# Kernel tuning notes

Hardware: AMD Instinct MI355X
Metric: run time of the kernel (lower is better)

Reference implementation:

```python
import jax, jax.numpy as jnp
import numpy as np

L = 512
INPUT = 1024
HIDDEN = 2048
VOCAB = 50257


def setup_inputs() -> dict:
    key = jax.random.key(0)
    ks = jax.random.split(key, 16)
    s_in = 1.0 / np.sqrt(INPUT)
    s_h = 1.0 / np.sqrt(HIDDEN)
    s_v = 1.0 / np.sqrt(VOCAB)
    f32 = jnp.float32
    return {
        "src": jax.random.normal(ks[0], (L, INPUT), f32),
        "tgt": jax.random.normal(ks[1], (L, INPUT), f32),
        # encoder LSTMCell params (torch layout: [4H, in], gate order i,f,g,o)
        "W_ih_e": jax.random.uniform(ks[2], (4 * HIDDEN, INPUT), f32, -s_h, s_h),
        "W_hh_e": jax.random.uniform(ks[3], (4 * HIDDEN, HIDDEN), f32, -s_h, s_h),
        "b_ih_e": jax.random.uniform(ks[4], (4 * HIDDEN,), f32, -s_h, s_h),
        "b_hh_e": jax.random.uniform(ks[5], (4 * HIDDEN,), f32, -s_h, s_h),
        # decoder LSTMCell params
        "W_ih_d": jax.random.uniform(ks[6], (4 * HIDDEN, INPUT), f32, -s_h, s_h),
        "W_hh_d": jax.random.uniform(ks[7], (4 * HIDDEN, HIDDEN), f32, -s_h, s_h),
        "b_ih_d": jax.random.uniform(ks[8], (4 * HIDDEN,), f32, -s_h, s_h),
        "b_hh_d": jax.random.uniform(ks[9], (4 * HIDDEN,), f32, -s_h, s_h),
        # fc_out: hidden -> vocab
        "W_out": jax.random.uniform(ks[10], (VOCAB, HIDDEN), f32, -s_h, s_h),
        "b_out": jax.random.uniform(ks[11], (VOCAB,), f32, -s_h, s_h),
        # fc_input_size: vocab -> input (computed per-step in original; unused under teacher forcing)
        "W_in": jax.random.uniform(ks[12], (INPUT, VOCAB), f32, -s_v, s_v),
        "b_in": jax.random.uniform(ks[13], (INPUT,), f32, -s_v, s_v),
    }


def _lstm_cell(x, h, c, W_ih, W_hh, b_ih, b_hh):
    # torch LSTMCell: gates split in order i, f, g, o
    gates = W_ih @ x + b_ih + W_hh @ h + b_hh  # [4H]
    i, f, g, o = jnp.split(gates, 4)
    i = jax.nn.sigmoid(i)
    f = jax.nn.sigmoid(f)
    g = jnp.tanh(g)
    o = jax.nn.sigmoid(o)
    c_new = f * c + i * g
    h_new = o * jnp.tanh(c_new)
    return h_new, c_new


def reference(src, tgt, W_ih_e, W_hh_e, b_ih_e, b_hh_e,
              W_ih_d, W_hh_d, b_ih_d, b_hh_d, W_out, b_out, W_in, b_in):
    H = W_hh_e.shape[1]

    # Encoder: run LSTMCell over src, keep final (h, c) as memory.
    def enc_step(carry, x):
        h, c = carry
        h, c = _lstm_cell(x, h, c, W_ih_e, W_hh_e, b_ih_e, b_hh_e)
        return (h, c), None

    h0 = jnp.zeros((H,), src.dtype)
    c0 = jnp.zeros((H,), src.dtype)
    memory, _ = jax.lax.scan(enc_step, (h0, c0), src)

    # Decoder (teacher forcing, free_running_rate=0.0): input is always tgt[i].
    def dec_step(carry, x):
        h, c = carry
        h, c = _lstm_cell(x, h, c, W_ih_d, W_hh_d, b_ih_d, b_hh_d)
        out = W_out @ h + b_out  # [vocab]
        return (h, c), out

    _, y = jax.lax.scan(dec_step, memory, tgt)  # [L, vocab]
    return y
```

## Files before the change

### kernel.cpp

```cpp
#include <hip/hip_runtime.h>

#define LSEQ 512
#define NIN 1024
#define NH 2048
#define NV 50257
#define NG 8192

typedef float f32x4 __attribute__((ext_vector_type(4)));
typedef short s16x8 __attribute__((ext_vector_type(8)));
typedef unsigned long long u64;

__device__ __forceinline__ unsigned short bf16_hi_rne(float x)
{
    unsigned u = __float_as_uint(x);
    return (unsigned short)((u + 0x7fffu + ((u >> 16) & 1u)) >> 16);
}

__global__ __launch_bounds__(256, 2)
void gemm_mfma_abT(const float* __restrict__ A, const float* __restrict__ B,
                   const float* __restrict__ bias1, const float* __restrict__ bias2,
                   float* __restrict__ C, int M, int N, int K)
{
    __shared__ unsigned short Ah[128 * 40], Al[128 * 40];
    __shared__ unsigned short Bh[128 * 40], Bl[128 * 40];

    const int tid  = threadIdx.x;
    const int m0   = blockIdx.x * 128;
    const int n0   = blockIdx.y * 128;
    const int lrow = tid >> 1;
    const int lk0  = (tid & 1) << 4;
    const int lane = tid & 63;
    const int wave = tid >> 6;
    const int wm   = (wave >> 1) * 64;
    const int wn   = (wave & 1) * 64;
    const int fr   = lane & 15;
    const int fk   = (lane >> 4) * 8;

    f32x4 acc[4][4];
#pragma unroll
    for (int i = 0; i < 4; ++i)
#pragma unroll
        for (int j = 0; j < 4; ++j) acc[i][j] = (f32x4){0.f, 0.f, 0.f, 0.f};

    const bool bvalid = (n0 + lrow) < N;
    const float* pa = A + (size_t)(m0 + lrow) * K + lk0;
    const float* pb = bvalid ? (B + (size_t)(n0 + lrow) * K + lk0) : nullptr;

    for (int k0 = 0; k0 < K; k0 += 32) {
        float4 va[4], vb[4];
#pragma unroll
        for (int q = 0; q < 4; ++q) va[q] = *(const float4*)(pa + k0 + 4 * q);
        if (bvalid) {
#pragma unroll
            for (int q = 0; q < 4; ++q) vb[q] = *(const float4*)(pb + k0 + 4 * q);
        } else {
#pragma unroll
            for (int q = 0; q < 4; ++q) vb[q] = make_float4(0.f, 0.f, 0.f, 0.f);
        }

#pragma unroll
        for (int q = 0; q < 4; ++q) {
            const float av[4] = {va[q].x, va[q].y, va[q].z, va[q].w};
            const float bv[4] = {vb[q].x, vb[q].y, vb[q].z, vb[q].w};
            ushort4 ah, alo, bh, blo;
            unsigned short* ahp = (unsigned short*)&ah;
            unsigned short* alp = (unsigned short*)&alo;
            unsigned short* bhp = (unsigned short*)&bh;
            unsigned short* blp = (unsigned short*)&blo;
#pragma unroll
            for (int j = 0; j < 4; ++j) {
                const unsigned short h = bf16_hi_rne(av[j]);
                ahp[j] = h;
                alp[j] = bf16_hi_rne(av[j] - __uint_as_float((unsigned)h << 16));
                const unsigned short g = bf16_hi_rne(bv[j]);
                bhp[j] = g;
                blp[j] = bf16_hi_rne(bv[j] - __uint_as_float((unsigned)g << 16));
            }
            const int sidx = lrow * 40 + lk0 + 4 * q;
            *(ushort4*)&Ah[sidx] = ah;
            *(ushort4*)&Al[sidx] = alo;
            *(ushort4*)&Bh[sidx] = bh;
            *(ushort4*)&Bl[sidx] = blo;
        }
        __syncthreads();

        s16x8 fah[4], fal[4], fbh[4], fbl[4];
#pragma unroll
        for (int i = 0; i < 4; ++i) {
            const int ar = (wm + i * 16 + fr) * 40 + fk;
            fah[i] = *(const s16x8*)&Ah[ar];
            fal[i] = *(const s16x8*)&Al[ar];
            const int br = (wn + i * 16 + fr) * 40 + fk;
            fbh[i] = *(const s16x8*)&Bh[br];
            fbl[i] = *(const s16x8*)&Bl[br];
        }
#pragma unroll
        for (int i = 0; i < 4; ++i)
#pragma unroll
            for (int j = 0; j < 4; ++j) {
                acc[i][j] = __builtin_amdgcn_mfma_f32_16x16x32_bf16(fah[i], fbh[j], acc[i][j], 0, 0, 0);
                acc[i][j] = __builtin_amdgcn_mfma_f32_16x16x32_bf16(fah[i], fbl[j], acc[i][j], 0, 0, 0);
                acc[i][j] = __builtin_amdgcn_mfma_f32_16x16x32_bf16(fal[i], fbh[j], acc[i][j], 0, 0, 0);
            }
        __syncthreads();
    }

    const int rbase = (lane >> 4) * 4;
#pragma unroll
    for (int j = 0; j < 4; ++j) {
        const int col = n0 + wn + j * 16 + fr;
        if (col >= N) continue;
        const float bb = bias1[col] + (bias2 ? bias2[col] : 0.f);
#pragma unroll
        for (int i = 0; i < 4; ++i) {
#pragma unroll
            for (int r = 0; r < 4; ++r) {
                const int row = m0 + wm + i * 16 + rbase + r;
                C[(size_t)row * N + col] = acc[i][j][r] + bb;
            }
        }
    }
}

__device__ __forceinline__ float sigmoidf_(float x)
{
    return 1.f / (1.f + __expf(-x));
}

__device__ __forceinline__ void tag_wait4(const u64* p0, const u64* p1,
                                          const u64* p2, const u64* p3,
                                          unsigned want, float* o)
{
    u64 a = __hip_atomic_load(p0, __ATOMIC_RELAXED, __HIP_MEMORY_SCOPE_AGENT);
    u64 b = __hip_atomic_load(p1, __ATOMIC_RELAXED, __HIP_MEMORY_SCOPE_AGENT);
    u64 c = __hip_atomic_load(p2, __ATOMIC_RELAXED, __HIP_MEMORY_SCOPE_AGENT);
    u64 d = __hip_atomic_load(p3, __ATOMIC_RELAXED, __HIP_MEMORY_SCOPE_AGENT);
    while (((unsigned)(a >> 32) != want) | ((unsigned)(b >> 32) != want) |
           ((unsigned)(c >> 32) != want) | ((unsigned)(d >> 32) != want)) {
        __builtin_amdgcn_s_sleep(1);
        a = __hip_atomic_load(p0, __ATOMIC_RELAXED, __HIP_MEMORY_SCOPE_AGENT);
        b = __hip_atomic_load(p1, __ATOMIC_RELAXED, __HIP_MEMORY_SCOPE_AGENT);
        c = __hip_atomic_load(p2, __ATOMIC_RELAXED, __HIP_MEMORY_SCOPE_AGENT);
        d = __hip_atomic_load(p3, __ATOMIC_RELAXED, __HIP_MEMORY_SCOPE_AGENT);
    }
    o[0] = __uint_as_float((unsigned)a);
    o[1] = __uint_as_float((unsigned)b);
    o[2] = __uint_as_float((unsigned)c);
    o[3] = __uint_as_float((unsigned)d);
}

#define W_LIST(F) F(0) F(1) F(2) F(3) F(4) F(5) F(6) F(7) F(8) F(9) F(10) F(11) \
  F(12) F(13) F(14) F(15) F(16) F(17) F(18) F(19) F(20) F(21) F(22) F(23) \
  F(24) F(25) F(26) F(27) F(28) F(29) F(30) F(31)
#define DECLW(I) f32x4 w##I;
#define LOADW(I) w##I = wp4[I];
#define PINW(I)  asm volatile("" : "+v"(w##I));

#define CHUNK(CH, WA, WB, WC, WD) do { \
    const f32x4 ha = *(const f32x4*)&h_s[hbase + (CH) * 16 + 0]; \
    const f32x4 hcb = *(const f32x4*)&h_s[hbase + (CH) * 16 + 4]; \
    const f32x4 hcc = *(const f32x4*)&h_s[hbase + (CH) * 16 + 8]; \
    const f32x4 hcd = *(const f32x4*)&h_s[hbase + (CH) * 16 + 12]; \
    p0 = fmaf(WA.x, ha.x, p0);  p0 = fmaf(WA.y, ha.y, p0); \
    p0 = fmaf(WA.z, ha.z, p0);  p0 = fmaf(WA.w, ha.w, p0); \
    p1 = fmaf(WB.x, hcb.x, p1); p1 = fmaf(WB.y, hcb.y, p1); \
    p1 = fmaf(WB.z, hcb.z, p1); p1 = fmaf(WB.w, hcb.w, p1); \
    p2 = fmaf(WC.x, hcc.x, p2); p2 = fmaf(WC.y, hcc.y, p2); \
    p2 = fmaf(WC.z, hcc.z, p2); p2 = fmaf(WC.w, hcc.w, p2); \
    p3 = fmaf(WD.x, hcd.x, p3); p3 = fmaf(WD.y, hcd.y, p3); \
    p3 = fmaf(WD.z, hcd.z, p3); p3 = fmaf(WD.w, hcd.w, p3); \
} while (0)

#define STEP(XP, T, GS, LAST, STOREHD) do { \
    float xc = 0.f; \
    if (sub == 0) xc = (XP)[(size_t)(T) * NG + grow];   \
    { \
        const u64* hsrc = hbq + ((GS) & 1) * NH; \
        float hv[4]; \
        tag_wait4(&hsrc[tid], &hsrc[tid + 512], &hsrc[tid + 1024], &hsrc[tid + 1536], \
                  (unsigned)((GS) + 1), hv); \
        h_s[tid          + ((tid          >> 7) << 2)] = hv[0]; \
        h_s[(tid +  512) + (((tid +  512) >> 7) << 2)] = hv[1]; \
        h_s[(tid + 1024) + (((tid + 1024) >> 7) << 2)] = hv[2]; \
        h_s[(tid + 1536) + (((tid + 1536) >> 7) << 2)] = hv[3]; \
    } \
    __syncthreads(); \
    float p0 = 0.f, p1 = 0.f, p2 = 0.f, p3 = 0.f; \
    CHUNK(0, w0, w1, w2, w3);     CHUNK(1, w4, w5, w6, w7); \
    CHUNK(2, w8, w9, w10, w11);   CHUNK(3, w12, w13, w14, w15); \
    CHUNK(4, w16, w17, w18, w19); CHUNK(5, w20, w21, w22, w23); \
    CHUNK(6, w24, w25, w26, w27); CHUNK(7, w28, w29, w30, w31); \
    float partial = (p0 + p1) + (p2 + p3); \
    partial += __shfl_xor(partial, 1); \
    partial += __shfl_xor(partial, 2); \
    partial += __shfl_xor(partial, 4); \
    partial += __shfl_xor(partial, 8); \
    if (sub == 0) gates_s[row] = partial + xc; \
    __syncthreads(); \
    if (tid < 8) { \
        const float ig = sigmoidf_(gates_s[tid]); \
        const float fg = sigmoidf_(gates_s[8 + tid]); \
        const float gg = tanhf(gates_s[16 + tid]); \
        const float og = sigmoidf_(gates_s[24 + tid]); \
        const float cn = fg * c_s[tid] + ig * gg; \
        c_s[tid] = cn; \
        const float hn = og * tanhf(cn); \
        if (STOREHD) Hd[(size_t)(T) * NH + wg * 8 + tid] = hn; \
        if (!(LAST)) { \
            const u64 pv = ((u64)(unsigned)((GS) + 2) << 32) | (u64)__float_as_uint(hn); \
            __hip_atomic_store(&hbq[(((GS) + 1) & 1) * NH + wg * 8 + tid], pv, \
                               __ATOMIC_RELAXED, __HIP_MEMORY_SCOPE_AGENT); \
        } \
    } \
} while (0)

__global__ __launch_bounds__(512, 2)
void seq_lstm(const float* __restrict__ Whh_e,
              const float* __restrict__ Whh_d,
              const float* __restrict__ Xe,
              const float* __restrict__ Xd,
              u64* __restrict__ hbq,
              float* __restrict__ Hd)
{
    const int wg   = blockIdx.x;
    const int tid  = threadIdx.x;
    const int lane = tid & 63;
    const int wv   = tid >> 6;
    const int row  = (wv << 2) + (lane >> 4);
    const int sub  = lane & 15;
    const int gate = row >> 3;
    const int u    = row & 7;
    const int grow = gate * NH + wg * 8 + u;
    const int hbase = sub * 132;

    __shared__ float h_s[2112];
    __shared__ float gates_s[32];
    __shared__ float c_s[8];

    W_LIST(DECLW)

    {
        const f32x4* wp4 = (const f32x4*)(Whh_e + (size_t)grow * NH + sub * 128);
        W_LIST(LOADW)
        W_LIST(PINW)
    }

    if (tid < 8) {
        c_s[tid] = 0.f;
        const u64 v0 = ((u64)1 << 32);
        __hip_atomic_store(&hbq[wg * 8 + tid], v0,
                           __ATOMIC_RELAXED, __HIP_MEMORY_SCOPE_AGENT);
    }
    __syncthreads();

#pragma unroll 1
    for (int t = 0; t < LSEQ; ++t) {
        STEP(Xe, t, t, false, false);
    }

    {
        const f32x4* wp4 = (const f32x4*)(Whh_d + (size_t)grow * NH + sub * 128);
        W_LIST(LOADW)
        W_LIST(PINW)
    }

#pragma unroll 1
    for (int t = 0; t < LSEQ; ++t) {
        STEP(Xd, t, LSEQ + t, (t == LSEQ - 1), true);
    }
}

extern "C" void kernel_launch(void* const* d_in, const int* in_sizes, int n_in,
                              void* d_out, int out_size, void* d_ws, size_t ws_size,
                              hipStream_t stream)
{
    const float* src   = (const float*)d_in[0];
    const float* tgt   = (const float*)d_in[1];
    const float* Wih_e = (const float*)d_in[2];
    const float* Whh_e = (const float*)d_in[3];
    const float* bih_e = (const float*)d_in[4];
    const float* bhh_e = (const float*)d_in[5];
    const float* Wih_d = (const float*)d_in[6];
    const float* Whh_d = (const float*)d_in[7];
    const float* bih_d = (const float*)d_in[8];
    const float* bhh_d = (const float*)d_in[9];
    const float* Wout  = (const float*)d_in[10];
    const float* bout  = (const float*)d_in[11];
    float* out = (float*)d_out;

    char* ws = (char*)d_ws;
    u64*  hbq = (u64*)ws;
    float* Hd = (float*)(ws + 32768);
    float* Xe = (float*)(ws + 32768 + (size_t)LSEQ * NH * 4);
    float* Xd = Xe + (size_t)LSEQ * NG;

    hipMemsetAsync(ws, 0, 32768, stream);

    const dim3 blk(256);
    gemm_mfma_abT<<<dim3(LSEQ / 128, NG / 128), blk, 0, stream>>>(
        src, Wih_e, bih_e, bhh_e, Xe, LSEQ, NG, NIN);
    gemm_mfma_abT<<<dim3(LSEQ / 128, NG / 128), blk, 0, stream>>>(
        tgt, Wih_d, bih_d, bhh_d, Xd, LSEQ, NG, NIN);

    seq_lstm<<<dim3(256), dim3(512), 0, stream>>>(
        Whh_e, Whh_d, Xe, Xd, hbq, Hd);

    gemm_mfma_abT<<<dim3(LSEQ / 128, (NV + 127) / 128), blk, 0, stream>>>(
        Hd, Wout, bout, nullptr, out, LSEQ, NV, NH);
}
```

Measured before the change: 3.212 ms.

## Remap rows so each wave owns one hidden unit, drop second barrier per step

Rows are remapped so each wavefront holds all four gates (i,f,g,o) of a single hidden unit. The gate nonlinearities are then computed in-wave through shuffles, with the cell state kept in a register instead of shared memory. This removes the gates_s shared-memory round trip and the second __syncthreads per recurrent step. The h staging buffer in LDS is double-buffered by step parity so the next step's writes cannot race with current reads, at the cost of twice the LDS and redundant activation math across lanes.

```diff
diff --git a/kernel.cpp b/kernel.cpp
--- a/kernel.cpp
+++ b/kernel.cpp
@@ -157,10 +157,10 @@
 #define PINW(I)  asm volatile("" : "+v"(w##I));
 
 #define CHUNK(CH, WA, WB, WC, WD) do { \
-    const f32x4 ha = *(const f32x4*)&h_s[hbase + (CH) * 16 + 0]; \
-    const f32x4 hcb = *(const f32x4*)&h_s[hbase + (CH) * 16 + 4]; \
-    const f32x4 hcc = *(const f32x4*)&h_s[hbase + (CH) * 16 + 8]; \
-    const f32x4 hcd = *(const f32x4*)&h_s[hbase + (CH) * 16 + 12]; \
+    const f32x4 ha = *(const f32x4*)&hb_s[hbase + (CH) * 16 + 0]; \
+    const f32x4 hcb = *(const f32x4*)&hb_s[hbase + (CH) * 16 + 4]; \
+    const f32x4 hcc = *(const f32x4*)&hb_s[hbase + (CH) * 16 + 8]; \
+    const f32x4 hcd = *(const f32x4*)&hb_s[hbase + (CH) * 16 + 12]; \
     p0 = fmaf(WA.x, ha.x, p0);  p0 = fmaf(WA.y, ha.y, p0); \
     p0 = fmaf(WA.z, ha.z, p0);  p0 = fmaf(WA.w, ha.w, p0); \
     p1 = fmaf(WB.x, hcb.x, p1); p1 = fmaf(WB.y, hcb.y, p1); \
@@ -172,19 +172,20 @@
 } while (0)
 
 #define STEP(XP, T, GS, LAST, STOREHD) do { \
-    float xc = 0.f; \
-    if (sub == 0) xc = (XP)[(size_t)(T) * NG + grow];   \
+    const float xc = (XP)[(size_t)(T) * NG + qg * NH + idx_u];  \
     { \
         const u64* hsrc = hbq + ((GS) & 1) * NH; \
         float hv[4]; \
         tag_wait4(&hsrc[tid], &hsrc[tid + 512], &hsrc[tid + 1024], &hsrc[tid + 1536], \
                   (unsigned)((GS) + 1), hv); \
-        h_s[tid          + ((tid          >> 7) << 2)] = hv[0]; \
-        h_s[(tid +  512) + (((tid +  512) >> 7) << 2)] = hv[1]; \
-        h_s[(tid + 1024) + (((tid + 1024) >> 7) << 2)] = hv[2]; \
-        h_s[(tid + 1536) + (((tid + 1536) >> 7) << 2)] = hv[3]; \
+        float* hst = h_s + ((GS) & 1) * 2112; \
+        hst[tid          + ((tid          >> 7) << 2)] = hv[0]; \
+        hst[(tid +  512) + (((tid +  512) >> 7) << 2)] = hv[1]; \
+        hst[(tid + 1024) + (((tid + 1024) >> 7) << 2)] = hv[2]; \
+        hst[(tid + 1536) + (((tid + 1536) >> 7) << 2)] = hv[3]; \
     } \
     __syncthreads(); \
+    const float* hb_s = h_s + ((GS) & 1) * 2112; \
     float p0 = 0.f, p1 = 0.f, p2 = 0.f, p3 = 0.f; \
     CHUNK(0, w0, w1, w2, w3);     CHUNK(1, w4, w5, w6, w7); \
     CHUNK(2, w8, w9, w10, w11);   CHUNK(3, w12, w13, w14, w15); \
@@ -195,20 +196,22 @@
     partial += __shfl_xor(partial, 2); \
     partial += __shfl_xor(partial, 4); \
     partial += __shfl_xor(partial, 8); \
-    if (sub == 0) gates_s[row] = partial + xc; \
-    __syncthreads(); \
-    if (tid < 8) { \
-        const float ig = sigmoidf_(gates_s[tid]); \
-        const float fg = sigmoidf_(gates_s[8 + tid]); \
-        const float gg = tanhf(gates_s[16 + tid]); \
-        const float og = sigmoidf_(gates_s[24 + tid]); \
-        const float cn = fg * c_s[tid] + ig * gg; \
-        c_s[tid] = cn; \
-        const float hn = og * tanhf(cn); \
-        if (STOREHD) Hd[(size_t)(T) * NH + wg * 8 + tid] = hn; \
+    const float gv = partial + xc; \
+    const float vi = __shfl(gv, sub,      64); \
+    const float vf = __shfl(gv, sub + 16, 64); \
+    const float vg = __shfl(gv, sub + 32, 64); \
+    const float vo = __shfl(gv, sub + 48, 64); \
+    const float ig = sigmoidf_(vi); \
+    const float fg = sigmoidf_(vf); \
+    const float gg = tanhf(vg); \
+    const float og = sigmoidf_(vo); \
+    c_reg = fg * c_reg + ig * gg; \
+    const float hn = og * tanhf(c_reg); \
+    if (lane == 0) { \
+        if (STOREHD) Hd[(size_t)(T) * NH + idx_u] = hn; \
         if (!(LAST)) { \
             const u64 pv = ((u64)(unsigned)((GS) + 2) << 32) | (u64)__float_as_uint(hn); \
-            __hip_atomic_store(&hbq[(((GS) + 1) & 1) * NH + wg * 8 + tid], pv, \
+            __hip_atomic_store(&hbq[(((GS) + 1) & 1) * NH + idx_u], pv, \
                                __ATOMIC_RELAXED, __HIP_MEMORY_SCOPE_AGENT); \
         } \
     } \
@@ -222,33 +225,30 @@
               u64* __restrict__ hbq,
               float* __restrict__ Hd)
 {
-    const int wg   = blockIdx.x;
-    const int tid  = threadIdx.x;
-    const int lane = tid & 63;
-    const int wv   = tid >> 6;
-    const int row  = (wv << 2) + (lane >> 4);
-    const int sub  = lane & 15;
-    const int gate = row >> 3;
-    const int u    = row & 7;
-    const int grow = gate * NH + wg * 8 + u;
+    const int wg    = blockIdx.x;
+    const int tid   = threadIdx.x;
+    const int lane  = tid & 63;
+    const int wv    = tid >> 6;
+    const int idx_u = wg * 8 + wv;
+    const int qg    = lane >> 4;
+    const int sub   = lane & 15;
     const int hbase = sub * 132;
 
-    __shared__ float h_s[2112];
-    __shared__ float gates_s[32];
-    __shared__ float c_s[8];
+    __shared__ float h_s[2 * 2112];
 
     W_LIST(DECLW)
 
     {
-        const f32x4* wp4 = (const f32x4*)(Whh_e + (size_t)grow * NH + sub * 128);
+        const f32x4* wp4 = (const f32x4*)(Whh_e + (size_t)(qg * NH + idx_u) * NH + sub * 128);
         W_LIST(LOADW)
         W_LIST(PINW)
     }
 
-    if (tid < 8) {
-        c_s[tid] = 0.f;
+    float c_reg = 0.f;
+
+    if (lane == 0) {
         const u64 v0 = ((u64)1 << 32);
-        __hip_atomic_store(&hbq[wg * 8 + tid], v0,
+        __hip_atomic_store(&hbq[idx_u], v0,
                            __ATOMIC_RELAXED, __HIP_MEMORY_SCOPE_AGENT);
     }
     __syncthreads();
@@ -259,7 +259,7 @@
     }
 
     {
-        const f32x4* wp4 = (const f32x4*)(Whh_d + (size_t)grow * NH + sub * 128);
+        const f32x4* wp4 = (const f32x4*)(Whh_d + (size_t)(qg * NH + idx_u) * NH + sub * 128);
         W_LIST(LOADW)
         W_LIST(PINW)
     }
```

After: 6.629 ms. +106.4%, slower.

## Use two-term bf16 split and double-buffered LDS in output projection GEMM

Applied to the files above, without the earlier changes.

Adds a dedicated output-projection GEMM that drops the A-low bf16 term, doing two MFMAs per tile instead of three. It also double-buffers LDS so the next tile's global loads and bf16 conversion overlap the current MFMAs. This cuts matrix work and conversion cost in the largest GEMM, but hidden-state values are now rounded to a single bf16, which lowers accuracy. The input-projection GEMMs keep the three-term kernel.

```diff
diff --git a/kernel.cpp b/kernel.cpp
--- a/kernel.cpp
+++ b/kernel.cpp
@@ -17,9 +17,9 @@
 }
 
 __global__ __launch_bounds__(256, 2)
-void gemm_mfma_abT(const float* __restrict__ A, const float* __restrict__ B,
-                   const float* __restrict__ bias1, const float* __restrict__ bias2,
-                   float* __restrict__ C, int M, int N, int K)
+void gemm_x3(const float* __restrict__ A, const float* __restrict__ B,
+             const float* __restrict__ bias1, const float* __restrict__ bias2,
+             float* __restrict__ C, int M, int N, int K)
 {
     __shared__ unsigned short Ah[128 * 40], Al[128 * 40];
     __shared__ unsigned short Bh[128 * 40], Bl[128 * 40];
@@ -111,6 +111,124 @@
         const int col = n0 + wn + j * 16 + fr;
         if (col >= N) continue;
         const float bb = bias1[col] + (bias2 ? bias2[col] : 0.f);
+#pragma unroll
+        for (int i = 0; i < 4; ++i) {
+#pragma unroll
+            for (int r = 0; r < 4; ++r) {
+                const int row = m0 + wm + i * 16 + rbase + r;
+                C[(size_t)row * N + col] = acc[i][j][r] + bb;
+            }
+        }
+    }
+}
+
+#define LOADG_O(K0) do { \
+    _Pragma("unroll") \
+    for (int q = 0; q < 4; ++q) va[q] = *(const float4*)(pa + (K0) + 4 * q); \
+    if (bvalid) { \
+        _Pragma("unroll") \
+        for (int q = 0; q < 4; ++q) vb[q] = *(const float4*)(pb + (K0) + 4 * q); \
+    } else { \
+        _Pragma("unroll") \
+        for (int q = 0; q < 4; ++q) vb[q] = make_float4(0.f, 0.f, 0.f, 0.f); \
+    } \
+} while (0)
+
+#define STORE_O(BUF) do { \
+    _Pragma("unroll") \
+    for (int q = 0; q < 4; ++q) { \
+        const float av[4] = {va[q].x, va[q].y, va[q].z, va[q].w}; \
+        const float bv[4] = {vb[q].x, vb[q].y, vb[q].z, vb[q].w}; \
+        ushort4 ah, bh, bl; \
+        unsigned short* ahp = (unsigned short*)&ah; \
+        unsigned short* bhp = (unsigned short*)&bh; \
+        unsigned short* blp = (unsigned short*)&bl; \
+        _Pragma("unroll") \
+        for (int j = 0; j < 4; ++j) { \
+            ahp[j] = bf16_hi_rne(av[j]); \
+            const unsigned short g = bf16_hi_rne(bv[j]); \
+            bhp[j] = g; \
+            blp[j] = bf16_hi_rne(bv[j] - __uint_as_float((unsigned)g << 16)); \
+        } \
+        const int sidx = lrow * 40 + lk0 + 4 * q; \
+        *(ushort4*)&Ah[BUF][sidx] = ah; \
+        *(ushort4*)&Bh[BUF][sidx] = bh; \
+        *(ushort4*)&Bl[BUF][sidx] = bl; \
+    } \
+} while (0)
+
+#define MFMA_O(BUF) do { \
+    s16x8 fah[4], fbh[4], fbl[4]; \
+    _Pragma("unroll") \
+    for (int i = 0; i < 4; ++i) { \
+        const int ar = (wm + i * 16 + fr) * 40 + fk; \
+        fah[i] = *(const s16x8*)&Ah[BUF][ar]; \
+        const int br = (wn + i * 16 + fr) * 40 + fk; \
+        fbh[i] = *(const s16x8*)&Bh[BUF][br]; \
+        fbl[i] = *(const s16x8*)&Bl[BUF][br]; \
+    } \
+    _Pragma("unroll") \
+    for (int i = 0; i < 4; ++i) \
+        _Pragma("unroll") \
+        for (int j = 0; j < 4; ++j) { \
+            acc[i][j] = __builtin_amdgcn_mfma_f32_16x16x32_bf16(fah[i], fbh[j], acc[i][j], 0, 0, 0); \
+            acc[i][j] = __builtin_amdgcn_mfma_f32_16x16x32_bf16(fah[i], fbl[j], acc[i][j], 0, 0, 0); \
+        } \
+} while (0)
+
+__global__ __launch_bounds__(256, 2)
+void gemm_out2(const float* __restrict__ A, const float* __restrict__ B,
+               const float* __restrict__ bias1,
+               float* __restrict__ C, int M, int N, int K)
+{
+    __shared__ unsigned short Ah[2][128 * 40];
+    __shared__ unsigned short Bh[2][128 * 40];
+    __shared__ unsigned short Bl[2][128 * 40];
+
+    const int tid  = threadIdx.x;
+    const int m0   = blockIdx.x * 128;
+    const int n0   = blockIdx.y * 128;
+    const int lrow = tid >> 1;
+    const int lk0  = (tid & 1) << 4;
+    const int lane = tid & 63;
+    const int wave = tid >> 6;
+    const int wm   = (wave >> 1) * 64;
+    const int wn   = (wave & 1) * 64;
+    const int fr   = lane & 15;
+    const int fk   = (lane >> 4) * 8;
+
+    f32x4 acc[4][4];
+#pragma unroll
+    for (int i = 0; i < 4; ++i)
+#pragma unroll
+        for (int j = 0; j < 4; ++j) acc[i][j] = (f32x4){0.f, 0.f, 0.f, 0.f};
+
+    const bool bvalid = (n0 + lrow) < N;
+    const float* pa = A + (size_t)(m0 + lrow) * K + lk0;
+    const float* pb = bvalid ? (B + (size_t)(n0 + lrow) * K + lk0) : nullptr;
+
+    float4 va[4], vb[4];
+
+    LOADG_O(0);
+    STORE_O(0);
+    __syncthreads();
+
+    int cur = 0;
+    for (int k0 = 32; k0 < K; k0 += 32) {
+        LOADG_O(k0);
+        MFMA_O(cur);
+        STORE_O(cur ^ 1);
+        __syncthreads();
+        cur ^= 1;
+    }
+    MFMA_O(cur);
+
+    const int rbase = (lane >> 4) * 4;
+#pragma unroll
+    for (int j = 0; j < 4; ++j) {
+        const int col = n0 + wn + j * 16 + fr;
+        if (col >= N) continue;
+        const float bb = bias1[col];
 #pragma unroll
         for (int i = 0; i < 4; ++i) {
 #pragma unroll
@@ -297,14 +415,14 @@
     hipMemsetAsync(ws, 0, 32768, stream);
 
     const dim3 blk(256);
-    gemm_mfma_abT<<<dim3(LSEQ / 128, NG / 128), blk, 0, stream>>>(
+    gemm_x3<<<dim3(LSEQ / 128, NG / 128), blk, 0, stream>>>(
         src, Wih_e, bih_e, bhh_e, Xe, LSEQ, NG, NIN);
-    gemm_mfma_abT<<<dim3(LSEQ / 128, NG / 128), blk, 0, stream>>>(
+    gemm_x3<<<dim3(LSEQ / 128, NG / 128), blk, 0, stream>>>(
         tgt, Wih_d, bih_d, bhh_d, Xd, LSEQ, NG, NIN);
 
     seq_lstm<<<dim3(256), dim3(512), 0, stream>>>(
         Whh_e, Whh_d, Xe, Xd, hbq, Hd);
 
-    gemm_mfma_abT<<<dim3(LSEQ / 128, (NV + 127) / 128), blk, 0, stream>>>(
-        Hd, Wout, bout, nullptr, out, LSEQ, NV, NH);
-}
+    gemm_out2<<<dim3(LSEQ / 128, (NV + 127) / 128), blk, 0, stream>>>(
+        Hd, Wout, bout, out, LSEQ, NV, NH);
+}
```

Result: no change. 3.262 ms (+1.6%).

## Use single-pass bf16 MFMA for output projection with XCD-aware block mapping

Applied to the files above, without the earlier changes.

The vocab projection GEMM moves from the split-bf16 three-MFMA scheme (hi/lo compensation) to a single bf16 MFMA per tile, cutting the MFMA work and LDS traffic for the largest GEMM. A 1D grid is remapped so the four M-tiles sharing a W_out column tile go to the same XCD, which should improve L2 reuse of W_out. The trade-off is lower accuracy on the output logits, since only the bf16-rounded inputs are used.

```diff
diff --git a/kernel.cpp b/kernel.cpp
--- a/kernel.cpp
+++ b/kernel.cpp
@@ -17,9 +17,9 @@
 }
 
 __global__ __launch_bounds__(256, 2)
-void gemm_mfma_abT(const float* __restrict__ A, const float* __restrict__ B,
-                   const float* __restrict__ bias1, const float* __restrict__ bias2,
-                   float* __restrict__ C, int M, int N, int K)
+void gemm_x3(const float* __restrict__ A, const float* __restrict__ B,
+             const float* __restrict__ bias1, const float* __restrict__ bias2,
+             float* __restrict__ C, int M, int N, int K)
 {
     __shared__ unsigned short Ah[128 * 40], Al[128 * 40];
     __shared__ unsigned short Bh[128 * 40], Bl[128 * 40];
@@ -111,6 +111,104 @@
         const int col = n0 + wn + j * 16 + fr;
         if (col >= N) continue;
         const float bb = bias1[col] + (bias2 ? bias2[col] : 0.f);
+#pragma unroll
+        for (int i = 0; i < 4; ++i) {
+#pragma unroll
+            for (int r = 0; r < 4; ++r) {
+                const int row = m0 + wm + i * 16 + rbase + r;
+                C[(size_t)row * N + col] = acc[i][j][r] + bb;
+            }
+        }
+    }
+}
+
+__global__ __launch_bounds__(256, 2)
+void gemm_out1(const float* __restrict__ A, const float* __restrict__ B,
+               const float* __restrict__ bias1,
+               float* __restrict__ C, int M, int N, int K)
+{
+    const int d = blockIdx.x;
+    const int xcd = d & 7;
+    const int l   = d >> 3;
+    const int p   = xcd + 8 * (l >> 2);
+    const int mt  = l & 3;
+    if (p >= (N + 127) / 128) return;
+    const int m0 = mt * 128;
+    const int n0 = p * 128;
+
+    __shared__ unsigned short Ah[128 * 40];
+    __shared__ unsigned short Bh[128 * 40];
+
+    const int tid  = threadIdx.x;
+    const int lrow = tid >> 1;
+    const int lk0  = (tid & 1) << 4;
+    const int lane = tid & 63;
+    const int wave = tid >> 6;
+    const int wm   = (wave >> 1) * 64;
+    const int wn   = (wave & 1) * 64;
+    const int fr   = lane & 15;
+    const int fk   = (lane >> 4) * 8;
+
+    f32x4 acc[4][4];
+#pragma unroll
+    for (int i = 0; i < 4; ++i)
+#pragma unroll
+        for (int j = 0; j < 4; ++j) acc[i][j] = (f32x4){0.f, 0.f, 0.f, 0.f};
+
+    const bool bvalid = (n0 + lrow) < N;
+    const float* pa = A + (size_t)(m0 + lrow) * K + lk0;
+    const float* pb = bvalid ? (B + (size_t)(n0 + lrow) * K + lk0) : nullptr;
+
+    for (int k0 = 0; k0 < K; k0 += 32) {
+        float4 va[4], vb[4];
+#pragma unroll
+        for (int q = 0; q < 4; ++q) va[q] = *(const float4*)(pa + k0 + 4 * q);
+        if (bvalid) {
+#pragma unroll
+            for (int q = 0; q < 4; ++q) vb[q] = *(const float4*)(pb + k0 + 4 * q);
+        } else {
+#pragma unroll
+            for (int q = 0; q < 4; ++q) vb[q] = make_float4(0.f, 0.f, 0.f, 0.f);
+        }
+
+#pragma unroll
+        for (int q = 0; q < 4; ++q) {
+            const float av[4] = {va[q].x, va[q].y, va[q].z, va[q].w};
+            const float bv[4] = {vb[q].x, vb[q].y, vb[q].z, vb[q].w};
+            ushort4 ah, bh;
+            unsigned short* ahp = (unsigned short*)&ah;
+            unsigned short* bhp = (unsigned short*)&bh;
+#pragma unroll
+            for (int j = 0; j < 4; ++j) {
+                ahp[j] = bf16_hi_rne(av[j]);
+                bhp[j] = bf16_hi_rne(bv[j]);
+            }
+            const int sidx = lrow * 40 + lk0 + 4 * q;
+            *(ushort4*)&Ah[sidx] = ah;
+            *(ushort4*)&Bh[sidx] = bh;
+        }
+        __syncthreads();
+
+        s16x8 fah[4], fbh[4];
+#pragma unroll
+        for (int i = 0; i < 4; ++i) {
+            fah[i] = *(const s16x8*)&Ah[(wm + i * 16 + fr) * 40 + fk];
+            fbh[i] = *(const s16x8*)&Bh[(wn + i * 16 + fr) * 40 + fk];
+        }
+#pragma unroll
+        for (int i = 0; i < 4; ++i)
+#pragma unroll
+            for (int j = 0; j < 4; ++j)
+                acc[i][j] = __builtin_amdgcn_mfma_f32_16x16x32_bf16(fah[i], fbh[j], acc[i][j], 0, 0, 0);
+        __syncthreads();
+    }
+
+    const int rbase = (lane >> 4) * 4;
+#pragma unroll
+    for (int j = 0; j < 4; ++j) {
+        const int col = n0 + wn + j * 16 + fr;
+        if (col >= N) continue;
+        const float bb = bias1[col];
 #pragma unroll
         for (int i = 0; i < 4; ++i) {
 #pragma unroll
@@ -297,14 +395,14 @@
     hipMemsetAsync(ws, 0, 32768, stream);
 
     const dim3 blk(256);
-    gemm_mfma_abT<<<dim3(LSEQ / 128, NG / 128), blk, 0, stream>>>(
+    gemm_x3<<<dim3(LSEQ / 128, NG / 128), blk, 0, stream>>>(
         src, Wih_e, bih_e, bhh_e, Xe, LSEQ, NG, NIN);
-    gemm_mfma_abT<<<dim3(LSEQ / 128, NG / 128), blk, 0, stream>>>(
+    gemm_x3<<<dim3(LSEQ / 128, NG / 128), blk, 0, stream>>>(
         tgt, Wih_d, bih_d, bhh_d, Xd, LSEQ, NG, NIN);
 
     seq_lstm<<<dim3(256), dim3(512), 0, stream>>>(
         Whh_e, Whh_d, Xe, Xd, hbq, Hd);
 
-    gemm_mfma_abT<<<dim3(LSEQ / 128, (NV + 127) / 128), blk, 0, stream>>>(
-        Hd, Wout, bout, nullptr, out, LSEQ, NV, NH);
-}
+    gemm_out1<<<dim3(1600), blk, 0, stream>>>(
+        Hd, Wout, bout, out, LSEQ, NV, NH);
+}
```

Result: faster. 3.054 ms, median of 2 (-4.9%).
